# Performance work log

Measured on AMD Instinct MI355X. Metric: run time of the kernel, lower is better.

## Reference

```python
import jax, jax.numpy as jnp
import numpy as np

NU = 200000  # num users
NI = 200000  # num items
H = 64
L = 2
E = 4000000
P = 100000
EPS = 1e-5


def _seg_mean(msgs, dst, n):
    # msgs: [E, H] gathered source features, dst: [E] destination ids
    s = jax.ops.segment_sum(msgs, dst, num_segments=n)
    c = jax.ops.segment_sum(jnp.ones((msgs.shape[0],), msgs.dtype), dst, num_segments=n)
    return s / jnp.maximum(c, 1.0)[:, None]


def _bn(x, g, b, m, v):
    return (x - m) * jax.lax.rsqrt(v + EPS) * g + b


def setup_inputs() -> dict:
    key = jax.random.key(0)
    ks = jax.random.split(key, 12)
    s = 1.0 / np.sqrt(H)
    inp = {
        "edge_index": jax.random.randint(ks[0], (2, E), 0, NU),
        "edge_label_index": jax.random.randint(ks[1], (2, P), 0, NU),
        "user_emb": jax.random.normal(ks[2], (NU, H), jnp.float32) * 0.1,
        "item_emb": jax.random.normal(ks[3], (NI, H), jnp.float32) * 0.1,
        "u_ll_w": jax.random.normal(ks[4], (L, H, H), jnp.float32) * s,
        "u_ll_b": jnp.zeros((L, H), jnp.float32),
        "u_lr_w": jax.random.normal(ks[5], (L, H, H), jnp.float32) * s,
        "i_ll_w": jax.random.normal(ks[6], (L, H, H), jnp.float32) * s,
        "i_ll_b": jnp.zeros((L, H), jnp.float32),
        "i_lr_w": jax.random.normal(ks[7], (L, H, H), jnp.float32) * s,
        "u_bn_g": jnp.ones((L, H), jnp.float32),
        "u_bn_b": jnp.zeros((L, H), jnp.float32),
        "u_bn_m": jnp.zeros((L, H), jnp.float32),
        "u_bn_v": jnp.ones((L, H), jnp.float32),
        "i_bn_g": jnp.ones((L, H), jnp.float32),
        "i_bn_b": jnp.zeros((L, H), jnp.float32),
        "i_bn_m": jnp.zeros((L, H), jnp.float32),
        "i_bn_v": jnp.ones((L, H), jnp.float32),
        "fc1_w": jax.random.normal(ks[8], (2 * H, H), jnp.float32) * (1.0 / np.sqrt(2 * H)),
        "fc1_b": jnp.zeros((H,), jnp.float32),
        "fc2_w": jax.random.normal(ks[9], (H, 4), jnp.float32) * s,
        "fc2_b": jnp.zeros((4,), jnp.float32),
    }
    return inp


def reference(edge_index, edge_label_index, user_emb, item_emb,
              u_ll_w, u_ll_b, u_lr_w, i_ll_w, i_ll_b, i_lr_w,
              u_bn_g, u_bn_b, u_bn_m, u_bn_v,
              i_bn_g, i_bn_b, i_bn_m, i_bn_v,
              fc1_w, fc1_b, fc2_w, fc2_b):
    src, dst = edge_index[0], edge_index[1]  # user -> item edges
    user_x, item_x = user_emb, item_emb
    for l in range(L):
        # user update: aggregate item features along flipped edges (item->user)
        agg_u = _seg_mean(item_x[dst], src, NU)          # [NU, H]
        u_new = agg_u @ u_ll_w[l] + u_ll_b[l] + user_x @ u_lr_w[l]
        u_new = jax.nn.relu(_bn(u_new, u_bn_g[l], u_bn_b[l], u_bn_m[l], u_bn_v[l]))
        # item update: aggregate (old) user features along user->item edges
        agg_i = _seg_mean(user_x[src], dst, NI)          # [NI, H]
        i_new = agg_i @ i_ll_w[l] + i_ll_b[l] + item_x @ i_lr_w[l]
        i_new = jax.nn.relu(_bn(i_new, i_bn_g[l], i_bn_b[l], i_bn_m[l], i_bn_v[l]))
        user_x, item_x = u_new, i_new
    u_h = user_x[edge_label_index[0]]                    # [P, H]
    i_h = item_x[edge_label_index[1]]                    # [P, H]
    x = jnp.concatenate([u_h, i_h], axis=1)              # [P, 2H]
    x = jax.nn.relu(x @ fc1_w + fc1_b)
    return x @ fc2_w + fc2_b                             # [P, 4]
```

## Files before the change

### kernel.cpp

```cpp
#include <hip/hip_runtime.h>

#define NU 200000
#define NI 200000
#define NN 400000
#define H 64
#define NE 4000000
#define NP 100000
#define EPSF 1e-5f

#define BSH 9
#define BNODES 512
#define NB ((NN + BNODES - 1) / BNODES)
#define CAP 15104

#define PBLOCKS 512
#define EPB ((NE + PBLOCKS - 1) / PBLOCKS)

#define DUMMY 200000
#define NROW 200002

typedef unsigned short u16;
typedef __attribute__((ext_vector_type(8))) short bf16x8;
typedef __attribute__((ext_vector_type(4))) float f32x4;

__device__ __forceinline__ u16 f2bf(float f) {
    unsigned int b = __float_as_uint(f);
    b += 0x7FFFu + ((b >> 16) & 1u);
    return (u16)(b >> 16);
}


__global__ __launch_bounds__(256) void part1_kernel(
    const int* __restrict__ src, const int* __restrict__ dst,
    int* __restrict__ blkhist)
{
    __shared__ int hist[NB];
    int tid = threadIdx.x, blk = blockIdx.x;
    for (int i = tid; i < NB; i += 256) hist[i] = 0;
    __syncthreads();
    int e0 = blk * EPB, e1 = min(NE, e0 + EPB);
    for (int e = e0 + tid; e < e1; e += 256) {
        atomicAdd(&hist[src[e] >> BSH], 1);
        atomicAdd(&hist[(NU + dst[e]) >> BSH], 1);
    }
    __syncthreads();
    for (int i = tid; i < NB; i += 256)
        blkhist[(size_t)i * PBLOCKS + blk] = hist[i];
}

__global__ __launch_bounds__(256) void colscan_kernel(
    int* __restrict__ blkhist, int* __restrict__ g_bcnt)
{
    __shared__ int s[256];
    int b = blockIdx.x, tid = threadIdx.x;
    int* col = blkhist + (size_t)b * PBLOCKS;
    int v0 = col[2 * tid], v1 = col[2 * tid + 1];
    int ps = v0 + v1;
    s[tid] = ps;
    __syncthreads();
    for (int d = 1; d < 256; d <<= 1) {
        int t = (tid >= d) ? s[tid - d] : 0;
        __syncthreads();
        s[tid] += t;
        __syncthreads();
    }
    int ex = s[tid] - ps;
    col[2 * tid] = ex;
    col[2 * tid + 1] = ex + v0;
    if (tid == 255) g_bcnt[b] = s[255];
}

__global__ __launch_bounds__(256) void part2_kernel(
    const int* __restrict__ src, const int* __restrict__ dst,
    const int* __restrict__ blkhist, int* __restrict__ staging)
{
    __shared__ int cur[NB];
    int tid = threadIdx.x, blk = blockIdx.x;
    for (int i = tid; i < NB; i += 256)
        cur[i] = i * CAP + blkhist[(size_t)i * PBLOCKS + blk];
    __syncthreads();
    int e0 = blk * EPB, e1 = min(NE, e0 + EPB);
    for (int e = e0 + tid; e < e1; e += 256) {
        int s = src[e], d = dst[e];
        int p1 = atomicAdd(&cur[s >> BSH], 1);
        staging[p1] = ((s & (BNODES - 1)) << 18) | d;
        int gn = NU + d;
        int p2 = atomicAdd(&cur[gn >> BSH], 1);
        staging[p2] = ((gn & (BNODES - 1)) << 18) | s;
    }
}

__global__ __launch_bounds__(256) void bucket_fill_kernel(
    const int* __restrict__ g_bcnt, const int* __restrict__ staging,
    int* __restrict__ off, int* __restrict__ deg, int* __restrict__ adj)
{
    __shared__ int hist[BNODES];
    __shared__ int psum[256];
    __shared__ int adj_st[CAP];
    int tid = threadIdx.x;
    int b = blockIdx.x;
    int e0 = b * CAP;
    int cnt = g_bcnt[b];
    int node_base = b * BNODES;

    for (int i = tid; i < CAP; i += 256) adj_st[i] = DUMMY;
    hist[tid] = 0; hist[tid + 256] = 0;
    __syncthreads();
    for (int i = tid; i < cnt; i += 256)
        atomicAdd(&hist[staging[e0 + i] >> 18], 1);
    __syncthreads();

    int h0 = hist[2 * tid], h1 = hist[2 * tid + 1];
    int hp0 = (h0 + 7) & ~7, hp1 = (h1 + 7) & ~7;
    psum[tid] = hp0 + hp1;
    __syncthreads();
    for (int d = 1; d < 256; d <<= 1) {
        int t = (tid >= d) ? psum[tid - d] : 0;
        __syncthreads();
        psum[tid] += t;
        __syncthreads();
    }
    int ex0 = psum[tid] - (hp0 + hp1);
    int ex1 = ex0 + hp0;
    int n0 = node_base + 2 * tid;
    if (n0 < NN)     { off[n0]     = e0 + ex0; deg[n0]     = h0; }
    if (n0 + 1 < NN) { off[n0 + 1] = e0 + ex1; deg[n0 + 1] = h1; }
    __syncthreads();
    hist[2 * tid] = ex0; hist[2 * tid + 1] = ex1;
    __syncthreads();

    int ptotal = min(psum[255], CAP);

    for (int i = tid; i < cnt; i += 256) {
        int v = staging[e0 + i];
        int p = atomicAdd(&hist[v >> 18], 1);
        if (p < CAP) adj_st[p] = v & 0x3FFFF;
    }
    __syncthreads();
    for (int i = tid; i < ptotal; i += 256)
        adj[(size_t)b * CAP + i] = adj_st[i];
}

__global__ __launch_bounds__(256) void cvt_kernel(
    const float4* __restrict__ inU, const float4* __restrict__ inI,
    ushort4* __restrict__ outU, ushort4* __restrict__ outI,
    u16* __restrict__ f1, int n4)
{
    int tid = threadIdx.x;
    if (blockIdx.x == 0 && tid < 192) {
        int s = tid >> 5, wd = tid & 31;
        unsigned int* p = (unsigned int*)(f1 + (size_t)s * NROW * H + (size_t)DUMMY * H);
        p[wd] = 0u;
    }
    int i = blockIdx.x * 256 + tid;
    const float4* in;
    ushort4* out;
    if (i < n4) { in = inU; out = outU; }
    else        { in = inI; out = outI; i -= n4; if (i >= n4) return; }
    float4 v = in[i];
    ushort4 h;
    h.x = f2bf(v.x); h.y = f2bf(v.y); h.z = f2bf(v.z); h.w = f2bf(v.w);
    out[i] = h;
}

__global__ __launch_bounds__(256) void pull_update_kernel(
    const int* __restrict__ off, const int* __restrict__ deg,
    const int* __restrict__ adj,
    const u16* __restrict__ xu16, const u16* __restrict__ xi16,
    const u16* __restrict__ selfU, const u16* __restrict__ selfI,
    u16* __restrict__ outU, u16* __restrict__ outI,
    const u16* __restrict__ wcat,
    const float* __restrict__ scsh)
{
    __shared__ u16 sAgg[4][16][72];
    int tid = threadIdx.x;
    int wave = tid >> 6, lane = tid & 63;
    int gw = blockIdx.x * 4 + wave;
    bool isU = gw < (NU / 16);
    int node0 = (isU ? gw : gw - NU / 16) * 16;
    const u16* table = isU ? xi16 : xu16;
    const u16* selfx = isU ? selfU : selfI;
    u16* out         = isU ? outU : outI;
    const u16* wt      = wcat + (isU ? 0 : 64 * 128);
    const float* sc_p  = scsh + (isU ? 0 : 128);
    const float* sh_p  = sc_p + 64;
    int wbase = isU ? node0 : NU + node0;

    int offv = 0, degv = 0;
    if (lane < 16) { offv = off[wbase + lane]; degv = deg[wbase + lane]; }

    int fl = lane & 15;
    int rg = lane >> 4;

    for (int s = 0; s < 16; ++s) {
        int beg = __shfl(offv, s);
        int dg  = __shfl(degv, s);
        int pdeg = (dg + 7) & ~7;
        float a0 = 0.f, a1 = 0.f, a2 = 0.f, a3 = 0.f;
        for (int k0 = 0; k0 < pdeg; k0 += 64) {
            int nb = adj[beg + k0 + lane];
            int nkk = min(64, pdeg - k0);
            for (int t = 0; t < nkk; t += 8) {
                int ia = __shfl(nb, t + rg);
                int ib = __shfl(nb, t + 4 + rg);
                uint2 wa = *(const uint2*)&table[(size_t)ia * H + fl * 4];
                uint2 wb = *(const uint2*)&table[(size_t)ib * H + fl * 4];
                a0 += __uint_as_float(wa.x << 16);
                a1 += __uint_as_float(wa.x & 0xFFFF0000u);
                a2 += __uint_as_float(wa.y << 16);
                a3 += __uint_as_float(wa.y & 0xFFFF0000u);
                a0 += __uint_as_float(wb.x << 16);
                a1 += __uint_as_float(wb.x & 0xFFFF0000u);
                a2 += __uint_as_float(wb.y << 16);
                a3 += __uint_as_float(wb.y & 0xFFFF0000u);
            }
        }
        a0 += __shfl_xor(a0, 16); a0 += __shfl_xor(a0, 32);
        a1 += __shfl_xor(a1, 16); a1 += __shfl_xor(a1, 32);
        a2 += __shfl_xor(a2, 16); a2 += __shfl_xor(a2, 32);
        a3 += __shfl_xor(a3, 16); a3 += __shfl_xor(a3, 32);
        if (lane < 16) {
            float inv = 1.0f / fmaxf((float)dg, 1.0f);
            unsigned int lo = ((unsigned int)f2bf(a1 * inv) << 16) | f2bf(a0 * inv);
            unsigned int hi = ((unsigned int)f2bf(a3 * inv) << 16) | f2bf(a2 * inv);
            uint2 pk; pk.x = lo; pk.y = hi;
            *(uint2*)&sAgg[wave][s][lane * 4] = pk;
        }
    }

    int row = lane & 15, g = lane >> 4;
    const u16* xrow = selfx + (size_t)(node0 + row) * H + g * 8;
    bf16x8 a[4];
    a[0] = *(const bf16x8*)&sAgg[wave][row][g * 8];
    a[1] = *(const bf16x8*)&sAgg[wave][row][32 + g * 8];
    a[2] = *(const bf16x8*)(xrow);
    a[3] = *(const bf16x8*)(xrow + 32);

#pragma unroll
    for (int ct = 0; ct < 4; ++ct) {
        int feat = ct * 16 + row;
        const u16* wrow = wt + feat * 128 + g * 8;
        f32x4 acc = {0.f, 0.f, 0.f, 0.f};
#pragma unroll
        for (int kb = 0; kb < 4; ++kb) {
            bf16x8 b = *(const bf16x8*)(wrow + kb * 32);
            acc = __builtin_amdgcn_mfma_f32_16x16x32_bf16(a[kb], b, acc, 0, 0, 0);
        }
        float s = sc_p[feat], h = sh_p[feat];
#pragma unroll
        for (int r = 0; r < 4; ++r) {
            int node = node0 + g * 4 + r;
            float v = fmaxf(acc[r] * s + h, 0.f);
            out[(size_t)node * H + feat] = f2bf(v);
        }
    }
}

__global__ __launch_bounds__(256) void wcvt_kernel(
    const float* __restrict__ u_ll_w, const float* __restrict__ u_lr_w,
    const float* __restrict__ i_ll_w, const float* __restrict__ i_lr_w,
    const float* __restrict__ u_ll_b, const float* __restrict__ i_ll_b,
    const float* __restrict__ u_g, const float* __restrict__ u_b,
    const float* __restrict__ u_m, const float* __restrict__ u_v,
    const float* __restrict__ i_g, const float* __restrict__ i_b,
    const float* __restrict__ i_m, const float* __restrict__ i_v,
    u16* __restrict__ wcat, float* __restrict__ scsh)
{
    int idx = blockIdx.x * 256 + threadIdx.x;
    if (idx < 32768) {
        int k = idx & 127, f = (idx >> 7) & 63, t = (idx >> 13) & 1, l = idx >> 14;
        const float* W = t ? (k < 64 ? i_ll_w : i_lr_w)
                           : (k < 64 ? u_ll_w : u_lr_w);
        wcat[idx] = f2bf(W[l * 4096 + (k & 63) * 64 + f]);
    }
    if (idx < 512) {
        int j = idx & 63, half = (idx >> 6) & 1, t = (idx >> 7) & 1, l = idx >> 8;
        const float *g = t ? i_g : u_g, *b = t ? i_b : u_b;
        const float *m = t ? i_m : u_m, *v = t ? i_v : u_v;
        const float *bl = t ? i_ll_b : u_ll_b;
        float sc = g[l * 64 + j] * rsqrtf(v[l * 64 + j] + EPSF);
        scsh[idx] = half ? (bl[l * 64 + j] - m[l * 64 + j]) * sc + b[l * 64 + j]
                         : sc;
    }
}

__global__ __launch_bounds__(256) void mlp_kernel(
    const int* __restrict__ eli,
    const u16* __restrict__ xu16, const u16* __restrict__ xi16,
    const float* __restrict__ fc1w, const float* __restrict__ fc1b,
    const float* __restrict__ fc2w, const float* __restrict__ fc2b,
    float* __restrict__ out, int n)
{
    __shared__ float sW[32][68];
    __shared__ float sA[64][36];
    __shared__ float sH[64][68];
    __shared__ int   sid[128];
    __shared__ float sW2[256];
    int tid = threadIdx.x;
    int p0 = blockIdx.x * 64;
    if (tid < 128) {
        int p = p0 + (tid & 63);
        int side = tid >> 6;
        sid[tid] = (p < n) ? eli[side * NP + p] : -1;
    }
    sW2[tid] = fc2w[tid];
    __syncthreads();

    int jt = (tid & 15) * 4;
    int pt = (tid >> 4) * 4;
    float4 b4 = *(const float4*)&fc1b[jt];
    float acc[4][4];
#pragma unroll
    for (int i = 0; i < 4; ++i) {
        acc[i][0] = b4.x; acc[i][1] = b4.y; acc[i][2] = b4.z; acc[i][3] = b4.w;
    }

    for (int ch = 0; ch < 4; ++ch) {
        int k0 = ch * 32;
        const u16* tab = (ch < 2) ? xu16 : xi16;
        int idbase = (ch < 2) ? 0 : 64;
        int koff = (ch & 1) * 32;
        for (int idx = tid; idx < 64 * 16; idx += 256) {
            int r = idx >> 4, cp = idx & 15;
            int id = sid[idbase + r];
            unsigned int wv = (id >= 0)
                ? *(const unsigned int*)&tab[(size_t)id * H + koff + cp * 2] : 0u;
            sA[r][cp * 2]     = __uint_as_float(wv << 16);
            sA[r][cp * 2 + 1] = __uint_as_float(wv & 0xFFFF0000u);
        }
        for (int idx = tid; idx < 32 * 64; idx += 256) {
            int kk = idx >> 6, j = idx & 63;
            sW[kk][j] = fc1w[(k0 + kk) * 64 + j];
        }
        __syncthreads();
        for (int kk = 0; kk < 32; kk += 4) {
            float a[4][4];
#pragma unroll
            for (int i = 0; i < 4; ++i) {
                float4 t = *(const float4*)&sA[pt + i][kk];
                a[i][0] = t.x; a[i][1] = t.y; a[i][2] = t.z; a[i][3] = t.w;
            }
#pragma unroll
            for (int q = 0; q < 4; ++q) {
                float4 w = *(const float4*)&sW[kk + q][jt];
                float wv[4] = {w.x, w.y, w.z, w.w};
#pragma unroll
                for (int i = 0; i < 4; ++i)
#pragma unroll
                    for (int j = 0; j < 4; ++j)
                        acc[i][j] += a[i][q] * wv[j];
            }
        }
        __syncthreads();
    }

#pragma unroll
    for (int i = 0; i < 4; ++i)
#pragma unroll
        for (int j = 0; j < 4; ++j)
            sH[pt + i][jt + j] = fmaxf(acc[i][j], 0.f);
    __syncthreads();

    int pp = tid >> 2, c = tid & 3;
    float o = 0.f;
#pragma unroll
    for (int j = 0; j < 64; ++j) o += sH[pp][j] * sW2[j * 4 + c];
    int p = p0 + pp;
    if (p < n) out[(size_t)p * 4 + c] = o + fc2b[c];
}

extern "C" void kernel_launch(void* const* d_in, const int* in_sizes, int n_in,
                              void* d_out, int out_size, void* d_ws, size_t ws_size,
                              hipStream_t stream) {
    const int*   edge_index = (const int*)d_in[0];
    const int*   eli        = (const int*)d_in[1];
    const float* user_emb   = (const float*)d_in[2];
    const float* item_emb   = (const float*)d_in[3];
    const float* u_ll_w     = (const float*)d_in[4];
    const float* u_ll_b     = (const float*)d_in[5];
    const float* u_lr_w     = (const float*)d_in[6];
    const float* i_ll_w     = (const float*)d_in[7];
    const float* i_ll_b     = (const float*)d_in[8];
    const float* i_lr_w     = (const float*)d_in[9];
    const float* u_bn_g     = (const float*)d_in[10];
    const float* u_bn_b     = (const float*)d_in[11];
    const float* u_bn_m     = (const float*)d_in[12];
    const float* u_bn_v     = (const float*)d_in[13];
    const float* i_bn_g     = (const float*)d_in[14];
    const float* i_bn_b     = (const float*)d_in[15];
    const float* i_bn_m     = (const float*)d_in[16];
    const float* i_bn_v     = (const float*)d_in[17];
    const float* fc1_w      = (const float*)d_in[18];
    const float* fc1_b      = (const float*)d_in[19];
    const float* fc2_w      = (const float*)d_in[20];
    const float* fc2_b      = (const float*)d_in[21];
    float* out = (float*)d_out;

    const int* src = edge_index;
    const int* dst = edge_index + NE;

    const size_t S = (size_t)NROW * H;
    char* w = (char*)d_ws;
    u16* f1 = (u16*)w;          w += 6 * S * 2;
    int* adj    = (int*)w;      w += (size_t)NB * CAP * 4;
    int* off    = (int*)w;      w += (size_t)NN * 4;
    int* deg    = (int*)w;      w += (size_t)NN * 4;
    int* g_bcnt = (int*)w;      w += (size_t)NB * 4;
    u16* wcat   = (u16*)w;      w += (size_t)32768 * 2;
    float* scsh = (float*)w;    w += (size_t)512 * 4;

    u16* emb16_u = f1 + 0 * S;
    u16* emb16_i = f1 + 1 * S;
    u16* fin16_u = f1 + 0 * S;
    u16* fin16_i = f1 + 1 * S;
    u16* xA16_u  = f1 + 4 * S;
    u16* xA16_i  = f1 + 5 * S;
    int* staging = (int*)(f1 + 2 * S);
    int* blkhist = (int*)(f1 + 4 * S);

    part1_kernel<<<PBLOCKS, 256, 0, stream>>>(src, dst, blkhist);
    colscan_kernel<<<NB, 256, 0, stream>>>(blkhist, g_bcnt);
    part2_kernel<<<PBLOCKS, 256, 0, stream>>>(src, dst, blkhist, staging);
    bucket_fill_kernel<<<NB, 256, 0, stream>>>(g_bcnt, staging, off, deg, adj);

    const int n4 = NU * H / 4;
    cvt_kernel<<<(2 * n4 + 255) / 256, 256, 0, stream>>>(
        (const float4*)user_emb, (const float4*)item_emb,
        (ushort4*)emb16_u, (ushort4*)emb16_i, f1, n4);
    wcvt_kernel<<<128, 256, 0, stream>>>(
        u_ll_w, u_lr_w, i_ll_w, i_lr_w, u_ll_b, i_ll_b,
        u_bn_g, u_bn_b, u_bn_m, u_bn_v,
        i_bn_g, i_bn_b, i_bn_m, i_bn_v, wcat, scsh);

    const int pu_blocks = (NN / 16) / 4;

    pull_update_kernel<<<pu_blocks, 256, 0, stream>>>(
        off, deg, adj, emb16_u, emb16_i, emb16_u, emb16_i,
        xA16_u, xA16_i, wcat, scsh);

    pull_update_kernel<<<pu_blocks, 256, 0, stream>>>(
        off, deg, adj, xA16_u, xA16_i, xA16_u, xA16_i,
        fin16_u, fin16_i, wcat + 16384, scsh + 256);

    mlp_kernel<<<(NP + 63) / 64, 256, 0, stream>>>(
        eli, fin16_u, fin16_i, fc1_w, fc1_b, fc2_w, fc2_b, out, NP);
}
```

Before: 645.3 us.

## Split wave across two nodes in gather, software-pipeline loads, vectorize edge partition

The gather kernel now has each half-wave process a different destination node, so two nodes are aggregated concurrently. Each lane gathers four neighbor rows per step, and the next batch of loads is issued before the current one is accumulated, to raise memory-level parallelism. Lanes past a node's degree are masked to a dummy row, and the adjacency buffer gets tail padding for the over-read. The partition kernels read src/dst as int4 with EPB fixed at 7816, a multiple of 4, which relies on NE divisibility to cover all edges. The self-feature load is hoisted ahead of the aggregation.

```diff
diff --git a/kernel.cpp b/kernel.cpp
--- a/kernel.cpp
+++ b/kernel.cpp
@@ -14,7 +14,7 @@
 #define CAP 15104
 
 #define PBLOCKS 512
-#define EPB ((NE + PBLOCKS - 1) / PBLOCKS)
+#define EPB 7816
 
 #define DUMMY 200000
 #define NROW 200002
@@ -39,9 +39,13 @@
     for (int i = tid; i < NB; i += 256) hist[i] = 0;
     __syncthreads();
     int e0 = blk * EPB, e1 = min(NE, e0 + EPB);
-    for (int e = e0 + tid; e < e1; e += 256) {
-        atomicAdd(&hist[src[e] >> BSH], 1);
-        atomicAdd(&hist[(NU + dst[e]) >> BSH], 1);
+    for (int e = e0 + tid * 4; e + 4 <= e1; e += 1024) {
+        int4 s4 = *(const int4*)&src[e];
+        int4 d4 = *(const int4*)&dst[e];
+        atomicAdd(&hist[s4.x >> BSH], 1); atomicAdd(&hist[(NU + d4.x) >> BSH], 1);
+        atomicAdd(&hist[s4.y >> BSH], 1); atomicAdd(&hist[(NU + d4.y) >> BSH], 1);
+        atomicAdd(&hist[s4.z >> BSH], 1); atomicAdd(&hist[(NU + d4.z) >> BSH], 1);
+        atomicAdd(&hist[s4.w >> BSH], 1); atomicAdd(&hist[(NU + d4.w) >> BSH], 1);
     }
     __syncthreads();
     for (int i = tid; i < NB; i += 256)
@@ -80,13 +84,20 @@
         cur[i] = i * CAP + blkhist[(size_t)i * PBLOCKS + blk];
     __syncthreads();
     int e0 = blk * EPB, e1 = min(NE, e0 + EPB);
-    for (int e = e0 + tid; e < e1; e += 256) {
-        int s = src[e], d = dst[e];
-        int p1 = atomicAdd(&cur[s >> BSH], 1);
-        staging[p1] = ((s & (BNODES - 1)) << 18) | d;
-        int gn = NU + d;
-        int p2 = atomicAdd(&cur[gn >> BSH], 1);
-        staging[p2] = ((gn & (BNODES - 1)) << 18) | s;
+    for (int e = e0 + tid * 4; e + 4 <= e1; e += 1024) {
+        int4 s4 = *(const int4*)&src[e];
+        int4 d4 = *(const int4*)&dst[e];
+        int sv[4] = {s4.x, s4.y, s4.z, s4.w};
+        int dv[4] = {d4.x, d4.y, d4.z, d4.w};
+#pragma unroll
+        for (int q = 0; q < 4; ++q) {
+            int s = sv[q], d = dv[q];
+            int p1 = atomicAdd(&cur[s >> BSH], 1);
+            staging[p1] = ((s & (BNODES - 1)) << 18) | d;
+            int gn = NU + d;
+            int p2 = atomicAdd(&cur[gn >> BSH], 1);
+            staging[p2] = ((gn & (BNODES - 1)) << 18) | s;
+        }
     }
 }
 
@@ -186,55 +197,98 @@
     const float* sh_p  = sc_p + 64;
     int wbase = isU ? node0 : NU + node0;
 
+    int row = lane & 15, g = lane >> 4;
+    const u16* xrow = selfx + (size_t)(node0 + row) * H + g * 8;
+    bf16x8 a2 = *(const bf16x8*)(xrow);
+    bf16x8 a3 = *(const bf16x8*)(xrow + 32);
+
     int offv = 0, degv = 0;
     if (lane < 16) { offv = off[wbase + lane]; degv = deg[wbase + lane]; }
 
-    int fl = lane & 15;
-    int rg = lane >> 4;
-
-    for (int s = 0; s < 16; ++s) {
-        int beg = __shfl(offv, s);
-        int dg  = __shfl(degv, s);
-        int pdeg = (dg + 7) & ~7;
-        float a0 = 0.f, a1 = 0.f, a2 = 0.f, a3 = 0.f;
-        for (int k0 = 0; k0 < pdeg; k0 += 64) {
-            int nb = adj[beg + k0 + lane];
-            int nkk = min(64, pdeg - k0);
-            for (int t = 0; t < nkk; t += 8) {
-                int ia = __shfl(nb, t + rg);
-                int ib = __shfl(nb, t + 4 + rg);
-                uint2 wa = *(const uint2*)&table[(size_t)ia * H + fl * 4];
-                uint2 wb = *(const uint2*)&table[(size_t)ib * H + fl * 4];
-                a0 += __uint_as_float(wa.x << 16);
-                a1 += __uint_as_float(wa.x & 0xFFFF0000u);
-                a2 += __uint_as_float(wa.y << 16);
-                a3 += __uint_as_float(wa.y & 0xFFFF0000u);
-                a0 += __uint_as_float(wb.x << 16);
-                a1 += __uint_as_float(wb.x & 0xFFFF0000u);
-                a2 += __uint_as_float(wb.y << 16);
-                a3 += __uint_as_float(wb.y & 0xFFFF0000u);
+    int half = lane >> 5;
+    int hl   = lane & 31;
+    int fl   = hl & 15;
+    int rg   = hl >> 4;
+    int shb  = (half << 5) + rg;
+
+#define ACC4(w) \
+    a0 += __uint_as_float((w).x << 16); a1 += __uint_as_float((w).x & 0xFFFF0000u); \
+    a0 += __uint_as_float((w).y << 16); a1 += __uint_as_float((w).y & 0xFFFF0000u);
+
+    for (int p = 0; p < 8; ++p) {
+        int begA = __shfl(offv, 2 * p),     dgA = __shfl(degv, 2 * p);
+        int begB = __shfl(offv, 2 * p + 1), dgB = __shfl(degv, 2 * p + 1);
+        int pdA = (dgA + 7) & ~7, pdB = (dgB + 7) & ~7;
+        int myBeg = half ? begB : begA;
+        int myPd  = half ? pdB  : pdA;
+        int tmax  = max(pdA, pdB);
+        float a0 = 0.f, a1 = 0.f, a2f = 0.f, a3f = 0.f;
+        for (int k0 = 0; k0 < tmax; k0 += 32) {
+            int nb = adj[myBeg + k0 + hl];
+            int lim = min(32, tmax - k0);
+            uint2 c0, c1, c2, c3;
+            {
+                int i0 = __shfl(nb, shb + 0), i1 = __shfl(nb, shb + 2);
+                int i2 = __shfl(nb, shb + 4), i3 = __shfl(nb, shb + 6);
+                if (k0 + 0 + rg >= myPd) i0 = DUMMY;
+                if (k0 + 2 + rg >= myPd) i1 = DUMMY;
+                if (k0 + 4 + rg >= myPd) i2 = DUMMY;
+                if (k0 + 6 + rg >= myPd) i3 = DUMMY;
+                c0 = *(const uint2*)&table[(size_t)i0 * H + fl * 4];
+                c1 = *(const uint2*)&table[(size_t)i1 * H + fl * 4];
+                c2 = *(const uint2*)&table[(size_t)i2 * H + fl * 4];
+                c3 = *(const uint2*)&table[(size_t)i3 * H + fl * 4];
             }
-        }
-        a0 += __shfl_xor(a0, 16); a0 += __shfl_xor(a0, 32);
-        a1 += __shfl_xor(a1, 16); a1 += __shfl_xor(a1, 32);
-        a2 += __shfl_xor(a2, 16); a2 += __shfl_xor(a2, 32);
-        a3 += __shfl_xor(a3, 16); a3 += __shfl_xor(a3, 32);
-        if (lane < 16) {
-            float inv = 1.0f / fmaxf((float)dg, 1.0f);
+            for (int tt = 8; tt < lim; tt += 8) {
+                int i0 = __shfl(nb, shb + tt + 0), i1 = __shfl(nb, shb + tt + 2);
+                int i2 = __shfl(nb, shb + tt + 4), i3 = __shfl(nb, shb + tt + 6);
+                if (k0 + tt + 0 + rg >= myPd) i0 = DUMMY;
+                if (k0 + tt + 2 + rg >= myPd) i1 = DUMMY;
+                if (k0 + tt + 4 + rg >= myPd) i2 = DUMMY;
+                if (k0 + tt + 6 + rg >= myPd) i3 = DUMMY;
+                uint2 n0 = *(const uint2*)&table[(size_t)i0 * H + fl * 4];
+                uint2 n1 = *(const uint2*)&table[(size_t)i1 * H + fl * 4];
+                uint2 n2 = *(const uint2*)&table[(size_t)i2 * H + fl * 4];
+                uint2 n3 = *(const uint2*)&table[(size_t)i3 * H + fl * 4];
+                a0 += __uint_as_float(c0.x << 16); a1 += __uint_as_float(c0.x & 0xFFFF0000u);
+                a2f += __uint_as_float(c0.y << 16); a3f += __uint_as_float(c0.y & 0xFFFF0000u);
+                a0 += __uint_as_float(c1.x << 16); a1 += __uint_as_float(c1.x & 0xFFFF0000u);
+                a2f += __uint_as_float(c1.y << 16); a3f += __uint_as_float(c1.y & 0xFFFF0000u);
+                a0 += __uint_as_float(c2.x << 16); a1 += __uint_as_float(c2.x & 0xFFFF0000u);
+                a2f += __uint_as_float(c2.y << 16); a3f += __uint_as_float(c2.y & 0xFFFF0000u);
+                a0 += __uint_as_float(c3.x << 16); a1 += __uint_as_float(c3.x & 0xFFFF0000u);
+                a2f += __uint_as_float(c3.y << 16); a3f += __uint_as_float(c3.y & 0xFFFF0000u);
+                c0 = n0; c1 = n1; c2 = n2; c3 = n3;
+            }
+            a0 += __uint_as_float(c0.x << 16); a1 += __uint_as_float(c0.x & 0xFFFF0000u);
+            a2f += __uint_as_float(c0.y << 16); a3f += __uint_as_float(c0.y & 0xFFFF0000u);
+            a0 += __uint_as_float(c1.x << 16); a1 += __uint_as_float(c1.x & 0xFFFF0000u);
+            a2f += __uint_as_float(c1.y << 16); a3f += __uint_as_float(c1.y & 0xFFFF0000u);
+            a0 += __uint_as_float(c2.x << 16); a1 += __uint_as_float(c2.x & 0xFFFF0000u);
+            a2f += __uint_as_float(c2.y << 16); a3f += __uint_as_float(c2.y & 0xFFFF0000u);
+            a0 += __uint_as_float(c3.x << 16); a1 += __uint_as_float(c3.x & 0xFFFF0000u);
+            a2f += __uint_as_float(c3.y << 16); a3f += __uint_as_float(c3.y & 0xFFFF0000u);
+        }
+        a0 += __shfl_xor(a0, 16);
+        a1 += __shfl_xor(a1, 16);
+        a2f += __shfl_xor(a2f, 16);
+        a3f += __shfl_xor(a3f, 16);
+        int mydg = half ? dgB : dgA;
+        if (rg == 0) {
+            float inv = 1.0f / fmaxf((float)mydg, 1.0f);
             unsigned int lo = ((unsigned int)f2bf(a1 * inv) << 16) | f2bf(a0 * inv);
-            unsigned int hi = ((unsigned int)f2bf(a3 * inv) << 16) | f2bf(a2 * inv);
+            unsigned int hi = ((unsigned int)f2bf(a3f * inv) << 16) | f2bf(a2f * inv);
             uint2 pk; pk.x = lo; pk.y = hi;
-            *(uint2*)&sAgg[wave][s][lane * 4] = pk;
-        }
-    }
-
-    int row = lane & 15, g = lane >> 4;
-    const u16* xrow = selfx + (size_t)(node0 + row) * H + g * 8;
+            *(uint2*)&sAgg[wave][2 * p + half][fl * 4] = pk;
+        }
+    }
+#undef ACC4
+
     bf16x8 a[4];
     a[0] = *(const bf16x8*)&sAgg[wave][row][g * 8];
     a[1] = *(const bf16x8*)&sAgg[wave][row][32 + g * 8];
-    a[2] = *(const bf16x8*)(xrow);
-    a[3] = *(const bf16x8*)(xrow + 32);
+    a[2] = a2;
+    a[3] = a3;
 
 #pragma unroll
     for (int ct = 0; ct < 4; ++ct) {
@@ -402,7 +456,7 @@
     const size_t S = (size_t)NROW * H;
     char* w = (char*)d_ws;
     u16* f1 = (u16*)w;          w += 6 * S * 2;
-    int* adj    = (int*)w;      w += (size_t)NB * CAP * 4;
+    int* adj    = (int*)w;      w += ((size_t)NB * CAP + 128) * 4;
     int* off    = (int*)w;      w += (size_t)NN * 4;
     int* deg    = (int*)w;      w += (size_t)NN * 4;
     int* g_bcnt = (int*)w;      w += (size_t)NB * 4;
```

New measurement: 550.9 us. 14.6% less time.
